# Kernel optimization log

Hardware: AMD Instinct MI355X
Metric: run time of the kernel (lower is better)

## Reference

```python
import jax, jax.numpy as jnp
import numpy as np

B, N, K, D = 2, 32768, 16, 64
EPS = 1e-6

def setup_inputs() -> dict:
    key = jax.random.key(0)
    k1, k2, k3, k4, k5, k6 = jax.random.split(key, 6)
    coords = jax.random.normal(k1, (B, N, 3), dtype=jnp.float32)
    features = jax.random.normal(k2, (B, D, N, 1), dtype=jnp.float32)
    idx = jax.random.randint(k3, (B, N, K), 0, N, dtype=jnp.int32)
    dist = jax.random.uniform(k4, (B, N, K), dtype=jnp.float32)
    conv_w = jax.random.normal(k5, (D, 10), dtype=jnp.float32) * 0.3  # 1x1 conv weight
    conv_b = jax.random.normal(k6, (D,), dtype=jnp.float32) * 0.01
    bn_gamma = jnp.ones((D,), dtype=jnp.float32)
    bn_beta = jnp.zeros((D,), dtype=jnp.float32)
    return {"coords": coords, "features": features, "dist": dist,
            "conv_w": conv_w, "conv_b": conv_b,
            "bn_gamma": bn_gamma, "bn_beta": bn_beta, "idx": idx}

def reference(coords, features, dist, conv_w, conv_b, bn_gamma, bn_beta, idx):
    # gather neighbor coords: (B, N, K, 3)
    neighbors = jax.vmap(lambda c, i: c[i])(coords, idx)
    center = jnp.broadcast_to(coords[:, :, None, :], (B, N, K, 3))
    # relative-position encoding: center | neighbor | center-neighbor | dist -> 10 channels
    concat = jnp.concatenate([center, neighbors, center - neighbors, dist[..., None]], axis=-1)
    # 1x1 conv == channel matmul: (B,N,K,10) @ (D,10)^T -> (B,N,K,D)
    x = jnp.einsum('bnkc,dc->bnkd', concat, conv_w) + conv_b
    # BatchNorm2d in training mode: batch stats over (B,N,K) per channel, eps=1e-6
    mean = jnp.mean(x, axis=(0, 1, 2))
    var = jnp.var(x, axis=(0, 1, 2))
    x = (x - mean) * jax.lax.rsqrt(var + EPS) * bn_gamma + bn_beta
    x = jax.nn.relu(x)
    x = jnp.transpose(x, (0, 3, 1, 2))  # (B, D, N, K)
    feat = jnp.broadcast_to(features, (B, D, N, K))
    return jnp.concatenate([x, feat], axis=1)  # (B, 2D, N, K)
```

## Files before the change

### kernel.cpp

```cpp
#include <hip/hip_runtime.h>

#define BB 2
#define NN 32768
#define KK 16
#define DD 64
#define NC 10
#define NMOM 65
#define NBLK1 256
#define BN_EPS 1e-6
#define BNK ((size_t)BB * NN * KK)

__host__ __device__ __forceinline__ constexpr int pair_idx(int i, int j) {
    return 10 + i * 10 - (i * (i - 1)) / 2 + (j - i);
}

__global__ __launch_bounds__(256) void k_moments(
    const float* __restrict__ coords, const float* __restrict__ dist,
    const int* __restrict__ idx, float* __restrict__ partials)
{
    const int tid = threadIdx.x;
    const int bn = blockIdx.x * 256 + tid;
    const int b = bn >> 15;

    float acc[NMOM];
#pragma unroll
    for (int v = 0; v < NMOM; ++v) acc[v] = 0.f;

    const float cx = coords[(size_t)bn * 3 + 0];
    const float cy = coords[(size_t)bn * 3 + 1];
    const float cz = coords[(size_t)bn * 3 + 2];
    const float* cb = coords + (size_t)b * NN * 3;

    for (int k = 0; k < KK; ++k) {
        const int j = idx[(size_t)bn * KK + k];
        const float nx = cb[(size_t)j * 3 + 0];
        const float ny = cb[(size_t)j * 3 + 1];
        const float nz = cb[(size_t)j * 3 + 2];
        const float dd = dist[(size_t)bn * KK + k];
        const float c[NC] = {cx, cy, cz, nx, ny, nz, cx - nx, cy - ny, cz - nz, dd};
#pragma unroll
        for (int i = 0; i < NC; ++i) acc[i] += c[i];
#pragma unroll
        for (int i = 0; i < NC; ++i)
#pragma unroll
            for (int jj = i; jj < NC; ++jj)
                acc[pair_idx(i, jj)] += c[i] * c[jj];
    }

    __shared__ float red[4 * NMOM];
    const int lane = tid & 63, wave = tid >> 6;
#pragma unroll
    for (int v = 0; v < NMOM; ++v) {
        float x = acc[v];
        x += __shfl_down(x, 32);
        x += __shfl_down(x, 16);
        x += __shfl_down(x, 8);
        x += __shfl_down(x, 4);
        x += __shfl_down(x, 2);
        x += __shfl_down(x, 1);
        if (lane == 0) red[wave * NMOM + v] = x;
    }
    __syncthreads();
    if (tid < NMOM) {
        float p = red[tid] + red[NMOM + tid] + red[2 * NMOM + tid] + red[3 * NMOM + tid];
        partials[blockIdx.x * NMOM + tid] = p;
    }
}

__global__ __launch_bounds__(320) void k_finalize(
    const float* __restrict__ partials,
    const float* __restrict__ conv_w, const float* __restrict__ conv_b,
    const float* __restrict__ gamma, const float* __restrict__ beta,
    float* __restrict__ wscaled, float* __restrict__ bias2)
{
    __shared__ double part[4][NMOM];
    __shared__ double sums[NMOM];
    const int tid = threadIdx.x;
    const int g = tid / NMOM, m = tid % NMOM;
    if (g < 4) {
        double s = 0.0;
        for (int blk = g * 64; blk < (g + 1) * 64; ++blk)
            s += (double)partials[blk * NMOM + m];
        part[g][m] = s;
    }
    __syncthreads();
    if (tid < NMOM)
        sums[tid] = part[0][tid] + part[1][tid] + part[2][tid] + part[3][tid];
    __syncthreads();
    if (tid < DD) {
        const double cnt = (double)BB * NN * KK;
        double mm[NC], w[NC];
#pragma unroll
        for (int c = 0; c < NC; ++c) {
            mm[c] = sums[c] / cnt;
            w[c] = (double)conv_w[tid * NC + c];
        }
        const double bd = (double)conv_b[tid];
        double wm = 0.0;
#pragma unroll
        for (int c = 0; c < NC; ++c) wm += w[c] * mm[c];
        const double mean = wm + bd;
        double ex2 = bd * bd + 2.0 * bd * wm;
#pragma unroll
        for (int i = 0; i < NC; ++i)
#pragma unroll
            for (int j = i; j < NC; ++j) {
                const double Mij = sums[pair_idx(i, j)] / cnt;
                ex2 += (i == j ? 1.0 : 2.0) * w[i] * w[j] * Mij;
            }
        const double var = ex2 - mean * mean;
        const double scale = (double)gamma[tid] / sqrt(var + BN_EPS);
        bias2[tid] = (float)((double)beta[tid] + (bd - mean) * scale);
#pragma unroll
        for (int c = 0; c < NC; ++c)
            wscaled[tid * NC + c] = (float)(w[c] * scale);
    }
}

__global__ __launch_bounds__(256) void k_c(
    const float* __restrict__ coords, const float* __restrict__ dist,
    const int* __restrict__ idx, float* __restrict__ cbuf)
{
    const int t = blockIdx.x * 256 + threadIdx.x;
    const int e0 = t << 2;
    const int bn = e0 >> 4;
    const int k0 = e0 & 15;
    const int b = bn >> 15;

    const float* cc = coords + (size_t)bn * 3;
    const float cx = cc[0], cy = cc[1], cz = cc[2];
    const float* cb = coords + (size_t)b * NN * 3;

    const int4 j4 = *reinterpret_cast<const int4*>(idx + (size_t)bn * KK + k0);
    const float4 d4 = *reinterpret_cast<const float4*>(dist + (size_t)bn * KK + k0);
    const int js[4] = {j4.x, j4.y, j4.z, j4.w};
    const float dsv[4] = {d4.x, d4.y, d4.z, d4.w};

    float c[4][NC];
#pragma unroll
    for (int q = 0; q < 4; ++q) {
        const float* nc2 = cb + (size_t)js[q] * 3;
        const float nx = nc2[0], ny = nc2[1], nz = nc2[2];
        c[q][0] = cx; c[q][1] = cy; c[q][2] = cz;
        c[q][3] = nx; c[q][4] = ny; c[q][5] = nz;
        c[q][6] = cx - nx; c[q][7] = cy - ny; c[q][8] = cz - nz;
        c[q][9] = dsv[q];
    }
#pragma unroll
    for (int ch = 0; ch < NC; ++ch) {
        float4 v{c[0][ch], c[1][ch], c[2][ch], c[3][ch]};
        *reinterpret_cast<float4*>(&cbuf[(size_t)ch * BNK + e0]) = v;
    }
}

__global__ __launch_bounds__(256) void k_out(
    const float* __restrict__ cbuf, const float* __restrict__ features,
    const float* __restrict__ wscaled, const float* __restrict__ bias2,
    float* __restrict__ out)
{
    const int nc  = blockIdx.x & 127;
    const int ch2 = (blockIdx.x >> 7) & 127;
    const int b   = blockIdx.x >> 14;
    const int tid = threadIdx.x;
    const size_t plane = ((size_t)b * 2 * DD + ch2) * ((size_t)NN * KK);

    if (ch2 < DD) {
        const int d = ch2;
        float wv[NC];
#pragma unroll
        for (int ch = 0; ch < NC; ++ch) wv[ch] = wscaled[d * NC + ch];
        const float b2 = bias2[d];
        const size_t locbase = (size_t)nc * 256 * KK;
        const size_t ebase = (size_t)b * NN * KK + locbase;

#pragma unroll
        for (int j = 0; j < 4; ++j) {
            const size_t off = (size_t)(j * 1024 + tid * 4);
            float4 a{b2, b2, b2, b2};
#pragma unroll
            for (int ch = 0; ch < NC; ++ch) {
                const float4 cv = *reinterpret_cast<const float4*>(
                    &cbuf[(size_t)ch * BNK + ebase + off]);
                const float w = wv[ch];
                a.x += cv.x * w; a.y += cv.y * w;
                a.z += cv.z * w; a.w += cv.w * w;
            }
            a.x = fmaxf(a.x, 0.f); a.y = fmaxf(a.y, 0.f);
            a.z = fmaxf(a.z, 0.f); a.w = fmaxf(a.w, 0.f);
            *reinterpret_cast<float4*>(out + plane + locbase + off) = a;
        }
    } else {
        const int d = ch2 - DD;
        const float* fb = features + ((size_t)b * DD + d) * NN;
        const size_t locbase = (size_t)nc * 256 * KK;
#pragma unroll
        for (int j = 0; j < 4; ++j) {
            const int q = j * 256 + tid;
            const int n = nc * 256 + (q >> 2);
            const float f = fb[n];
            *reinterpret_cast<float4*>(out + plane + locbase + (size_t)q * 4) =
                float4{f, f, f, f};
        }
    }
}

extern "C" void kernel_launch(void* const* d_in, const int* in_sizes, int n_in,
                              void* d_out, int out_size, void* d_ws, size_t ws_size,
                              hipStream_t stream) {
    const float* coords   = (const float*)d_in[0];
    const float* features = (const float*)d_in[1];
    const float* dist     = (const float*)d_in[2];
    const float* conv_w   = (const float*)d_in[3];
    const float* conv_b   = (const float*)d_in[4];
    const float* gamma    = (const float*)d_in[5];
    const float* beta     = (const float*)d_in[6];
    const int*   idx      = (const int*)d_in[7];
    float* out = (float*)d_out;

    float* partials = (float*)d_ws;
    float* wscaled  = partials + NBLK1 * NMOM;
    float* bias2    = wscaled + DD * NC;
    float* cbuf     = (float*)d_ws + 65536;

    k_moments<<<NBLK1, 256, 0, stream>>>(coords, dist, idx, partials);
    k_finalize<<<1, 320, 0, stream>>>(partials, conv_w, conv_b, gamma, beta,
                                      wscaled, bias2);
    k_c<<<(int)(BNK / 4 / 256), 256, 0, stream>>>(coords, dist, idx, cbuf);
    k_out<<<BB * 128 * 128, 256, 0, stream>>>(cbuf, features, wscaled, bias2, out);
}
```

Baseline: 642.6 us.

## Fuse channel-buffer construction into output kernel and fold center weights algebraically

Drops the intermediate 10-channel buffer kernel and has the output kernel gather neighbor coords, idx and dist directly. Each thread handles one point across all K, and the center, neighbor and difference weights are folded so only 4 FMAs per element remain. This removes writing and then reading the 10-channel buffer, roughly 40 MB each way. In exchange every one of the 64 channel blocks now re-gathers idx, dist and neighbor coords, which depends on cache hits. Stores are now per-thread 64-byte rows, so they are less coalesced than before.

```diff
diff --git a/kernel.cpp b/kernel.cpp
--- a/kernel.cpp
+++ b/kernel.cpp
@@ -8,7 +8,6 @@
 #define NMOM 65
 #define NBLK1 256
 #define BN_EPS 1e-6
-#define BNK ((size_t)BB * NN * KK)
 
 __host__ __device__ __forceinline__ constexpr int pair_idx(int i, int j) {
     return 10 + i * 10 - (i * (i - 1)) / 2 + (j - i);
@@ -117,44 +116,9 @@
     }
 }
 
-__global__ __launch_bounds__(256) void k_c(
-    const float* __restrict__ coords, const float* __restrict__ dist,
-    const int* __restrict__ idx, float* __restrict__ cbuf)
-{
-    const int t = blockIdx.x * 256 + threadIdx.x;
-    const int e0 = t << 2;
-    const int bn = e0 >> 4;
-    const int k0 = e0 & 15;
-    const int b = bn >> 15;
-
-    const float* cc = coords + (size_t)bn * 3;
-    const float cx = cc[0], cy = cc[1], cz = cc[2];
-    const float* cb = coords + (size_t)b * NN * 3;
-
-    const int4 j4 = *reinterpret_cast<const int4*>(idx + (size_t)bn * KK + k0);
-    const float4 d4 = *reinterpret_cast<const float4*>(dist + (size_t)bn * KK + k0);
-    const int js[4] = {j4.x, j4.y, j4.z, j4.w};
-    const float dsv[4] = {d4.x, d4.y, d4.z, d4.w};
-
-    float c[4][NC];
-#pragma unroll
-    for (int q = 0; q < 4; ++q) {
-        const float* nc2 = cb + (size_t)js[q] * 3;
-        const float nx = nc2[0], ny = nc2[1], nz = nc2[2];
-        c[q][0] = cx; c[q][1] = cy; c[q][2] = cz;
-        c[q][3] = nx; c[q][4] = ny; c[q][5] = nz;
-        c[q][6] = cx - nx; c[q][7] = cy - ny; c[q][8] = cz - nz;
-        c[q][9] = dsv[q];
-    }
-#pragma unroll
-    for (int ch = 0; ch < NC; ++ch) {
-        float4 v{c[0][ch], c[1][ch], c[2][ch], c[3][ch]};
-        *reinterpret_cast<float4*>(&cbuf[(size_t)ch * BNK + e0]) = v;
-    }
-}
-
 __global__ __launch_bounds__(256) void k_out(
-    const float* __restrict__ cbuf, const float* __restrict__ features,
+    const float* __restrict__ coords, const float* __restrict__ features,
+    const float* __restrict__ dist, const int* __restrict__ idx,
     const float* __restrict__ wscaled, const float* __restrict__ bias2,
     float* __restrict__ out)
 {
@@ -170,24 +134,38 @@
 #pragma unroll
         for (int ch = 0; ch < NC; ++ch) wv[ch] = wscaled[d * NC + ch];
         const float b2 = bias2[d];
-        const size_t locbase = (size_t)nc * 256 * KK;
-        const size_t ebase = (size_t)b * NN * KK + locbase;
-
-#pragma unroll
-        for (int j = 0; j < 4; ++j) {
-            const size_t off = (size_t)(j * 1024 + tid * 4);
-            float4 a{b2, b2, b2, b2};
-#pragma unroll
-            for (int ch = 0; ch < NC; ++ch) {
-                const float4 cv = *reinterpret_cast<const float4*>(
-                    &cbuf[(size_t)ch * BNK + ebase + off]);
-                const float w = wv[ch];
-                a.x += cv.x * w; a.y += cv.y * w;
-                a.z += cv.z * w; a.w += cv.w * w;
+
+        const int n = nc * 256 + tid;
+        const int bn = b * NN + n;
+        const float* cc = coords + (size_t)bn * 3;
+        const float cx = cc[0], cy = cc[1], cz = cc[2];
+        const float* cb = coords + (size_t)b * NN * 3;
+
+        const float s_cen = b2 + (wv[0] + wv[6]) * cx + (wv[1] + wv[7]) * cy
+                               + (wv[2] + wv[8]) * cz;
+        const float a3 = wv[3] - wv[6], a4 = wv[4] - wv[7], a5 = wv[5] - wv[8];
+        const float a9 = wv[9];
+
+        const int4*   ip = reinterpret_cast<const int4*>(idx + (size_t)bn * KK);
+        const float4* dp = reinterpret_cast<const float4*>(dist + (size_t)bn * KK);
+        float* dst = out + plane + (size_t)n * KK;
+
+#pragma unroll
+        for (int kq = 0; kq < 4; ++kq) {
+            const int4 j4 = ip[kq];
+            const float4 d4 = dp[kq];
+            const int js[4] = {j4.x, j4.y, j4.z, j4.w};
+            const float dsv[4] = {d4.x, d4.y, d4.z, d4.w};
+            float4 r;
+            float* rp = reinterpret_cast<float*>(&r);
+#pragma unroll
+            for (int q = 0; q < 4; ++q) {
+                const float* nb = cb + (size_t)js[q] * 3;
+                const float v = s_cen + a3 * nb[0] + a4 * nb[1] + a5 * nb[2]
+                                      + a9 * dsv[q];
+                rp[q] = fmaxf(v, 0.f);
             }
-            a.x = fmaxf(a.x, 0.f); a.y = fmaxf(a.y, 0.f);
-            a.z = fmaxf(a.z, 0.f); a.w = fmaxf(a.w, 0.f);
-            *reinterpret_cast<float4*>(out + plane + locbase + off) = a;
+            *reinterpret_cast<float4*>(dst + kq * 4) = r;
         }
     } else {
         const int d = ch2 - DD;
@@ -220,11 +198,10 @@
     float* partials = (float*)d_ws;
     float* wscaled  = partials + NBLK1 * NMOM;
     float* bias2    = wscaled + DD * NC;
-    float* cbuf     = (float*)d_ws + 65536;
 
     k_moments<<<NBLK1, 256, 0, stream>>>(coords, dist, idx, partials);
     k_finalize<<<1, 320, 0, stream>>>(partials, conv_w, conv_b, gamma, beta,
                                       wscaled, bias2);
-    k_c<<<(int)(BNK / 4 / 256), 256, 0, stream>>>(coords, dist, idx, cbuf);
-    k_out<<<BB * 128 * 128, 256, 0, stream>>>(cbuf, features, wscaled, bias2, out);
-}
+    k_out<<<BB * 128 * 128, 256, 0, stream>>>(coords, features, dist, idx,
+                                              wscaled, bias2, out);
+}
```

Result: slower. 835.0 us (+29.9%).
